# Performance work log

Hardware: AMD Instinct MI355X
Metric: run time of the kernel (lower is better)

## Reference

```python
import jax, jax.numpy as jnp
import numpy as np

B, FIN, FOUT, FH2, NMIX, LAT, H, W = 16, 256, 256, 256, 8, 512, 64, 64


def _xavier(key, shape):
    # xavier_normal_ over last-two-ish dims; simple fan-based scale
    fan_in = int(np.prod(shape[1:]))
    fan_out = shape[0]
    s = (2.0 / (fan_in + fan_out)) ** 0.5
    return jax.random.normal(key, shape, jnp.float32) * s


def setup_inputs() -> dict:
    key = jax.random.key(0)
    ks = jax.random.split(key, 12)
    return {
        "x": jax.random.normal(ks[0], (B, FIN, H, W), jnp.float32),
        "lat": jax.random.normal(ks[1], (B, LAT), jnp.float32),
        # mixture kernel banks [n_mix, out_ch, in_ch] (kernel_size=1 squeezed)
        "k_in_mix": _xavier(ks[2], (NMIX, FH2, FIN)),
        "k_mid_mix": _xavier(ks[3], (NMIX, FH2, 2 * FH2)),
        "k_out_mix": _xavier(ks[4], (NMIX, FOUT, 2 * FH2)),
        "k_short_mix": _xavier(ks[5], (NMIX, FOUT, FIN)),
        # mixture bias banks [n_mix, ch]
        "b_in_mix": _xavier(ks[6], (NMIX, FH2)),
        "b_mid_mix": _xavier(ks[7], (NMIX, FH2)),
        "b_out_mix": _xavier(ks[8], (NMIX, FOUT)),
        "b_short_mix": _xavier(ks[9], (NMIX, FOUT)),
        # dyna_mix = nn.Linear(lat_size, n_mix) (lat_factor=0 path)
        "w_dyna": _xavier(ks[10], (NMIX, LAT)),
        "b_dyna": jnp.zeros((NMIX,), jnp.float32),
    }


def _complex_wave(h):
    # doubles channel dim: concat(sin, cos) along channels (per sample)
    return jnp.concatenate([jnp.sin(h), jnp.cos(h)], axis=1)


def reference(x, lat, k_in_mix, k_mid_mix, k_out_mix, k_short_mix,
              b_in_mix, b_mid_mix, b_out_mix, b_short_mix, w_dyna, b_dyna):
    # mixing coefficients per sample: [B, n_mix]
    mix = lat @ w_dyna.T + b_dyna
    # per-sample 1x1 conv kernels via mixture reduction: [B, out, in]
    k_in = jnp.einsum('bm,moi->boi', mix, k_in_mix)
    k_mid = jnp.einsum('bm,moi->boi', mix, k_mid_mix)
    k_out = jnp.einsum('bm,moi->boi', mix, k_out_mix)
    k_short = jnp.einsum('bm,moi->boi', mix, k_short_mix)
    # per-sample biases: [B, ch, 1, 1]
    b_in = (mix @ b_in_mix)[:, :, None, None]
    b_mid = (mix @ b_mid_mix)[:, :, None, None]
    b_out = (mix @ b_out_mix)[:, :, None, None]
    b_short = (mix @ b_short_mix)[:, :, None, None]
    # grouped conv with groups = batch (kernel_size=1) == per-sample matmul
    short = jnp.einsum('boi,bihw->bohw', k_short, x) + b_short
    h = jnp.einsum('boi,bihw->bohw', k_in, x) + b_in            # [B, FH2, H, W]
    h = _complex_wave(h)                                        # [B, 2*FH2, H, W]
    h = jnp.einsum('boi,bihw->bohw', k_mid, h) + b_mid
    h = _complex_wave(h)
    out = jnp.einsum('boi,bihw->bohw', k_out, h) + b_out + short
    return out
```

## Files before the change

### kernel.cpp

```cpp
#include <hip/hip_runtime.h>
#include <stdint.h>

#define B_    16
#define FIN   256
#define FOUT  256
#define FH2   256
#define NMIX  8
#define LAT   512
#define HW    4096
#define MT    64

typedef short bf16x8 __attribute__((ext_vector_type(8)));
typedef float f32x4  __attribute__((ext_vector_type(4)));

#define WS_MIX    0
#define WS_BIAS   1024
#define WS_WIN    131072
#define WS_WMID   2228224
#define WS_WOUT   6422528
#define WS_WSHORT 10616832

__device__ __forceinline__ uint16_t f2bf(float f) {
  uint32_t u = __builtin_bit_cast(uint32_t, f);
  u += 0x7fffu + ((u >> 16) & 1u);
  return (uint16_t)(u >> 16);
}
__device__ __forceinline__ uint32_t pack2(float lo, float hi) {
  return (uint32_t)f2bf(lo) | ((uint32_t)f2bf(hi) << 16);
}

#define MFMA(a, b, c) __builtin_amdgcn_mfma_f32_16x16x32_bf16(a, b, c, 0, 0, 0)

__global__ void k_mix_bias(const float* __restrict__ lat,
                           const float* __restrict__ w_dyna,
                           const float* __restrict__ b_dyna,
                           const float* __restrict__ b_in_mix,
                           const float* __restrict__ b_mid_mix,
                           const float* __restrict__ b_out_mix,
                           const float* __restrict__ b_short_mix,
                           float* __restrict__ ws_mix,
                           float* __restrict__ ws_bias) {
  __shared__ float smix[NMIX];
  const int t = threadIdx.x;
  const int lane = t & 63, wv = t >> 6;
  const int b = blockIdx.x;
#pragma unroll
  for (int d2 = 0; d2 < 2; d2++) {
    int m = wv * 2 + d2;
    float s = 0.f;
#pragma unroll
    for (int j = 0; j < 8; j++)
      s += lat[b * LAT + j * 64 + lane] * w_dyna[m * LAT + j * 64 + lane];
#pragma unroll
    for (int off = 32; off; off >>= 1) s += __shfl_xor(s, off);
    if (lane == 0) {
      float v = s + b_dyna[m];
      ws_mix[b * NMIX + m] = v;
      smix[m] = v;
    }
  }
  __syncthreads();
  const float* banks[4] = {b_in_mix, b_mid_mix, b_out_mix, b_short_mix};
  for (int pos = t; pos < 1024; pos += 256) {
    int bank = pos >> 8, ch = pos & 255;
    const float* bp = banks[bank];
    float a = 0.f;
#pragma unroll
    for (int m = 0; m < NMIX; m++) a += smix[m] * bp[m * 256 + ch];
    ws_bias[(bank * B_ + b) * 256 + ch] = a;
  }
}

__global__ void k_weights(const float* __restrict__ k_in_mix,
                          const float* __restrict__ k_mid_mix,
                          const float* __restrict__ k_out_mix,
                          const float* __restrict__ k_short_mix,
                          const float* __restrict__ ws_mix,
                          uint16_t* __restrict__ w_in,
                          uint16_t* __restrict__ w_mid,
                          uint16_t* __restrict__ w_out,
                          uint16_t* __restrict__ w_short) {
  __shared__ float smix[B_ * NMIX];
  const int t = threadIdx.x;
  if (t < B_ * NMIX) smix[t] = ws_mix[t];
  __syncthreads();
  const int idx = blockIdx.x * 256 + t;
  const float* src;
  uint16_t* dst;
  int sstride, dstride;
  if (idx < 65536) {
    int e = idx;
    int j = e & 7, lane = (e >> 3) & 63, ots = (e >> 9) & 3, kt = (e >> 11) & 7, wv = e >> 14;
    int row = wv * 64 + ots * 16 + (lane & 15);
    int k = kt * 32 + (lane >> 4) * 8 + j;
    src = k_in_mix + row * 256 + k; sstride = 65536;
    dst = w_in + e;                 dstride = 65536;
  } else if (idx < 196608) {
    int e = idx - 65536;
    int j = e & 7, lane = (e >> 3) & 63, ots = (e >> 9) & 3, kt = (e >> 11) & 15, wv = e >> 15;
    int row = wv * 64 + ots * 16 + (lane & 15);
    int kp = kt * 32 + (lane >> 4) * 8 + j;
    int i = (kp >> 1) + ((kp & 1) << 8);
    src = k_mid_mix + row * 512 + i; sstride = 131072;
    dst = w_mid + e;                 dstride = 131072;
  } else if (idx < 327680) {
    int e = idx - 196608;
    int j = e & 7, lane = (e >> 3) & 63, ots = (e >> 9) & 3, kt = (e >> 11) & 15, wv = e >> 15;
    int row = wv * 64 + ots * 16 + (lane & 15);
    int kp = kt * 32 + (lane >> 4) * 8 + j;
    int i = (kp >> 1) + ((kp & 1) << 8);
    src = k_out_mix + row * 512 + i; sstride = 131072;
    dst = w_out + e;                 dstride = 131072;
  } else {
    int e = idx - 327680;
    int j = e & 7, lane = (e >> 3) & 63, ots = (e >> 9) & 3, kt = (e >> 11) & 7, wv = e >> 14;
    int row = wv * 64 + ots * 16 + (lane & 15);
    int k = kt * 32 + (lane >> 4) * 8 + j;
    src = k_short_mix + row * 256 + k; sstride = 65536;
    dst = w_short + e;                 dstride = 65536;
  }
  float v[NMIX];
#pragma unroll
  for (int m = 0; m < NMIX; m++) v[m] = src[m * sstride];
  for (int b = 0; b < B_; b++) {
    float a = 0.f;
#pragma unroll
    for (int m = 0; m < NMIX; m++) a += smix[b * NMIX + m] * v[m];
    dst[b * dstride] = f2bf(a);
  }
}

__launch_bounds__(256, 2)
__global__ void k_main(const float* __restrict__ x,
                       const float* __restrict__ ws_bias,
                       const uint16_t* __restrict__ w_in,
                       const uint16_t* __restrict__ w_mid,
                       const uint16_t* __restrict__ w_out,
                       const uint16_t* __restrict__ w_short,
                       float* __restrict__ out) {
  __shared__ int4 smem4[73728 / 16];
  char* lds = (char*)smem4;
  char* Xc = lds;
  char* H1 = lds + 8192;

  const int t = threadIdx.x;
  const int lane = t & 63;
  const int wv = t >> 6;
  const int q = lane >> 4;
  const int n = lane & 15;
  const int b = blockIdx.x & 15;
  const int p0 = (blockIdx.x >> 4) * MT;

  const float* xb = x + (size_t)b * FIN * HW + p0;
  const int xpos = t & 63;
  const int xcg = wv;

  {
    const float* xs = xb + (size_t)(xcg * 8) * HW + xpos;
    float v[8];
#pragma unroll
    for (int e = 0; e < 8; e++) v[e] = xs[(size_t)e * HW];
    *(int4*)(Xc + xpos * 64 + ((xcg ^ (xpos & 3)) * 16)) =
        make_int4((int)pack2(v[0], v[1]), (int)pack2(v[2], v[3]),
                  (int)pack2(v[4], v[5]), (int)pack2(v[6], v[7]));
  }

  f32x4 acc_h[4][4], acc_s[4][4];
#pragma unroll
  for (int ots = 0; ots < 4; ots++) {
    const int o = wv * 64 + ots * 16 + q * 4;
    const float4 vi = *(const float4*)&ws_bias[(0 * B_ + b) * 256 + o];
    const float4 vs = *(const float4*)&ws_bias[(3 * B_ + b) * 256 + o];
    f32x4 ah, asv;
    ah[0] = vi.x; ah[1] = vi.y; ah[2] = vi.z; ah[3] = vi.w;
    asv[0] = vs.x; asv[1] = vs.y; asv[2] = vs.z; asv[3] = vs.w;
#pragma unroll
    for (int pt = 0; pt < 4; pt++) { acc_h[ots][pt] = ah; acc_s[ots][pt] = asv; }
  }

  const uint16_t* Wi = w_in + (size_t)b * 65536 + wv * 16384 + lane * 8;
  const uint16_t* Ws = w_short + (size_t)b * 65536 + wv * 16384 + lane * 8;
  bf16x8 ai[2][4], asf[2][4];
#pragma unroll
  for (int ots = 0; ots < 4; ots++) {
    ai[0][ots] = *(const bf16x8*)(Wi + ots * 512);
    asf[0][ots] = *(const bf16x8*)(Ws + ots * 512);
  }
  __syncthreads();

#pragma unroll
  for (int kt = 0; kt < 8; kt++) {
    float xv[8];
    if (kt < 7) {
      const float* xs = xb + (size_t)((kt + 1) * 32 + xcg * 8) * HW + xpos;
#pragma unroll
      for (int e = 0; e < 8; e++) xv[e] = xs[(size_t)e * HW];
#pragma unroll
      for (int ots = 0; ots < 4; ots++) {
        ai[(kt + 1) & 1][ots] = *(const bf16x8*)(Wi + (kt + 1) * 2048 + ots * 512);
        asf[(kt + 1) & 1][ots] = *(const bf16x8*)(Ws + (kt + 1) * 2048 + ots * 512);
      }
    }
    const char* Xr = Xc + (kt & 1) * 4096;
    bf16x8 bf[4];
#pragma unroll
    for (int pt = 0; pt < 4; pt++) {
      const int p = pt * 16 + n;
      bf[pt] = *(const bf16x8*)(Xr + p * 64 + ((q ^ (p & 3)) * 16));
    }
#pragma unroll
    for (int ots = 0; ots < 4; ots++) {
#pragma unroll
      for (int pt = 0; pt < 4; pt++) {
        acc_h[ots][pt] = MFMA(ai[kt & 1][ots], bf[pt], acc_h[ots][pt]);
        acc_s[ots][pt] = MFMA(asf[kt & 1][ots], bf[pt], acc_s[ots][pt]);
      }
    }
    if (kt < 7) {
      *(int4*)(Xc + ((kt + 1) & 1) * 4096 + xpos * 64 + ((xcg ^ (xpos & 3)) * 16)) =
          make_int4((int)pack2(xv[0], xv[1]), (int)pack2(xv[2], xv[3]),
                    (int)pack2(xv[4], xv[5]), (int)pack2(xv[6], xv[7]));
      __syncthreads();
    }
  }

#pragma unroll
  for (int ots = 0; ots < 4; ots++) {
    const int ctile = (wv * 4 + ots) * 4 + q;
#pragma unroll
    for (int pt = 0; pt < 4; pt++) {
      const int p = pt * 16 + n;
      *(int4*)(H1 + p * 1024 + ((ctile ^ (p & 7)) * 16)) = make_int4(
          (int)pack2(__sinf(acc_h[ots][pt][0]), __cosf(acc_h[ots][pt][0])),
          (int)pack2(__sinf(acc_h[ots][pt][1]), __cosf(acc_h[ots][pt][1])),
          (int)pack2(__sinf(acc_h[ots][pt][2]), __cosf(acc_h[ots][pt][2])),
          (int)pack2(__sinf(acc_h[ots][pt][3]), __cosf(acc_h[ots][pt][3])));
    }
  }

  const uint16_t* Wm = w_mid + (size_t)b * 131072 + wv * 32768 + lane * 8;
  bf16x8 am[3][4];
#pragma unroll
  for (int ots = 0; ots < 4; ots++) {
    am[0][ots] = *(const bf16x8*)(Wm + ots * 512);
    am[1][ots] = *(const bf16x8*)(Wm + 2048 + ots * 512);
  }
  f32x4 acc2[4][4];
#pragma unroll
  for (int ots = 0; ots < 4; ots++) {
    const int o = wv * 64 + ots * 16 + q * 4;
    const float4 v = *(const float4*)&ws_bias[(1 * B_ + b) * 256 + o];
    f32x4 a2;
    a2[0] = v.x; a2[1] = v.y; a2[2] = v.z; a2[3] = v.w;
#pragma unroll
    for (int pt = 0; pt < 4; pt++) acc2[ots][pt] = a2;
  }
  __syncthreads();

#pragma unroll
  for (int kt = 0; kt < 16; kt++) {
    if (kt < 14) {
#pragma unroll
      for (int ots = 0; ots < 4; ots++)
        am[(kt + 2) % 3][ots] = *(const bf16x8*)(Wm + (kt + 2) * 2048 + ots * 512);
    }
    bf16x8 bf[4];
#pragma unroll
    for (int pt = 0; pt < 4; pt++) {
      const int p = pt * 16 + n;
      bf[pt] = *(const bf16x8*)(H1 + p * 1024 + (((kt * 4 + q) ^ (p & 7)) * 16));
    }
#pragma unroll
    for (int ots = 0; ots < 4; ots++)
#pragma unroll
      for (int pt = 0; pt < 4; pt++)
        acc2[ots][pt] = MFMA(am[kt % 3][ots], bf[pt], acc2[ots][pt]);
  }
  __syncthreads();

#pragma unroll
  for (int ots = 0; ots < 4; ots++) {
    const int ctile = (wv * 4 + ots) * 4 + q;
#pragma unroll
    for (int pt = 0; pt < 4; pt++) {
      const int p = pt * 16 + n;
      *(int4*)(H1 + p * 1024 + ((ctile ^ (p & 7)) * 16)) = make_int4(
          (int)pack2(__sinf(acc2[ots][pt][0]), __cosf(acc2[ots][pt][0])),
          (int)pack2(__sinf(acc2[ots][pt][1]), __cosf(acc2[ots][pt][1])),
          (int)pack2(__sinf(acc2[ots][pt][2]), __cosf(acc2[ots][pt][2])),
          (int)pack2(__sinf(acc2[ots][pt][3]), __cosf(acc2[ots][pt][3])));
    }
  }

  const uint16_t* Wo = w_out + (size_t)b * 131072 + wv * 32768 + lane * 8;
  bf16x8 ao[3][4];
#pragma unroll
  for (int ots = 0; ots < 4; ots++) {
    ao[0][ots] = *(const bf16x8*)(Wo + ots * 512);
    ao[1][ots] = *(const bf16x8*)(Wo + 2048 + ots * 512);
  }
#pragma unroll
  for (int ots = 0; ots < 4; ots++) {
    const int o = wv * 64 + ots * 16 + q * 4;
    const float4 v = *(const float4*)&ws_bias[(2 * B_ + b) * 256 + o];
#pragma unroll
    for (int pt = 0; pt < 4; pt++) {
      acc_s[ots][pt][0] += v.x; acc_s[ots][pt][1] += v.y;
      acc_s[ots][pt][2] += v.z; acc_s[ots][pt][3] += v.w;
    }
  }
  __syncthreads();

#pragma unroll
  for (int kt = 0; kt < 16; kt++) {
    if (kt < 14) {
#pragma unroll
      for (int ots = 0; ots < 4; ots++)
        ao[(kt + 2) % 3][ots] = *(const bf16x8*)(Wo + (kt + 2) * 2048 + ots * 512);
    }
    bf16x8 bf[4];
#pragma unroll
    for (int pt = 0; pt < 4; pt++) {
      const int p = pt * 16 + n;
      bf[pt] = *(const bf16x8*)(H1 + p * 1024 + (((kt * 4 + q) ^ (p & 7)) * 16));
    }
#pragma unroll
    for (int ots = 0; ots < 4; ots++)
#pragma unroll
      for (int pt = 0; pt < 4; pt++)
        acc_s[ots][pt] = MFMA(ao[kt % 3][ots], bf[pt], acc_s[ots][pt]);
  }

  {
    float* ob = out + (size_t)b * FOUT * HW + p0;
#pragma unroll
    for (int ots = 0; ots < 4; ots++) {
#pragma unroll
      for (int pt = 0; pt < 4; pt++) {
#pragma unroll
        for (int r = 0; r < 4; r++) {
          const int o = wv * 64 + ots * 16 + q * 4 + r;
          ob[(size_t)o * HW + pt * 16 + n] = acc_s[ots][pt][r];
        }
      }
    }
  }
}

extern "C" void kernel_launch(void* const* d_in, const int* in_sizes, int n_in,
                              void* d_out, int out_size, void* d_ws, size_t ws_size,
                              hipStream_t stream) {
  const float* x           = (const float*)d_in[0];
  const float* lat         = (const float*)d_in[1];
  const float* k_in_mix    = (const float*)d_in[2];
  const float* k_mid_mix   = (const float*)d_in[3];
  const float* k_out_mix   = (const float*)d_in[4];
  const float* k_short_mix = (const float*)d_in[5];
  const float* b_in_mix    = (const float*)d_in[6];
  const float* b_mid_mix   = (const float*)d_in[7];
  const float* b_out_mix   = (const float*)d_in[8];
  const float* b_short_mix = (const float*)d_in[9];
  const float* w_dyna      = (const float*)d_in[10];
  const float* b_dyna      = (const float*)d_in[11];

  char* ws = (char*)d_ws;
  float*    ws_mix  = (float*)(ws + WS_MIX);
  float*    ws_bias = (float*)(ws + WS_BIAS);
  uint16_t* w_in    = (uint16_t*)(ws + WS_WIN);
  uint16_t* w_mid   = (uint16_t*)(ws + WS_WMID);
  uint16_t* w_out   = (uint16_t*)(ws + WS_WOUT);
  uint16_t* w_short = (uint16_t*)(ws + WS_WSHORT);
  float* out = (float*)d_out;

  hipLaunchKernelGGL(k_mix_bias, dim3(16), dim3(256), 0, stream,
                     lat, w_dyna, b_dyna, b_in_mix, b_mid_mix, b_out_mix,
                     b_short_mix, ws_mix, ws_bias);
  hipLaunchKernelGGL(k_weights, dim3(1536), dim3(256), 0, stream,
                     k_in_mix, k_mid_mix, k_out_mix, k_short_mix, ws_mix,
                     w_in, w_mid, w_out, w_short);
  hipLaunchKernelGGL(k_main, dim3(1024), dim3(256), 0, stream,
                     x, ws_bias, w_in, w_mid, w_out, w_short, out);
}
```

Baseline: 207.5 us.

## Vectorize weight mixing and deepen prefetch pipelines with MFMA priority

The weight-mixing kernel now has each thread process 8 contiguous packed outputs. It reads float4 vectors and writes int4 packets, which cuts the grid from 1536 to 192 blocks and removes scalar strided accesses. The main kernel prefetches x two k-tiles ahead instead of one, and deepens the w_mid and w_out register prefetch from 3 to 4 stages. It also wraps the MFMA blocks in s_setprio to favour the matrix issue. The cost is higher register pressure under the 2-blocks-per-SM launch bound, which could cause spills or lower occupancy.

```diff
diff --git a/kernel.cpp b/kernel.cpp
--- a/kernel.cpp
+++ b/kernel.cpp
@@ -84,49 +84,64 @@
   const int t = threadIdx.x;
   if (t < B_ * NMIX) smix[t] = ws_mix[t];
   __syncthreads();
-  const int idx = blockIdx.x * 256 + t;
-  const float* src;
+  const int e8 = (blockIdx.x * 256 + t) * 8;
+  const float* srcA;
   uint16_t* dst;
   int sstride, dstride;
-  if (idx < 65536) {
-    int e = idx;
-    int j = e & 7, lane = (e >> 3) & 63, ots = (e >> 9) & 3, kt = (e >> 11) & 7, wv = e >> 14;
+  bool ileave;
+  if (e8 < 65536) {
+    int e = e8;
+    int lane = (e >> 3) & 63, ots = (e >> 9) & 3, kt = (e >> 11) & 7, wv = e >> 14;
     int row = wv * 64 + ots * 16 + (lane & 15);
-    int k = kt * 32 + (lane >> 4) * 8 + j;
-    src = k_in_mix + row * 256 + k; sstride = 65536;
-    dst = w_in + e;                 dstride = 65536;
-  } else if (idx < 196608) {
-    int e = idx - 65536;
-    int j = e & 7, lane = (e >> 3) & 63, ots = (e >> 9) & 3, kt = (e >> 11) & 15, wv = e >> 15;
+    int k0 = kt * 32 + (lane >> 4) * 8;
+    srcA = k_in_mix + row * 256 + k0; sstride = 65536; ileave = false;
+    dst = w_in + e;                   dstride = 65536;
+  } else if (e8 < 196608) {
+    int e = e8 - 65536;
+    int lane = (e >> 3) & 63, ots = (e >> 9) & 3, kt = (e >> 11) & 15, wv = e >> 15;
     int row = wv * 64 + ots * 16 + (lane & 15);
-    int kp = kt * 32 + (lane >> 4) * 8 + j;
-    int i = (kp >> 1) + ((kp & 1) << 8);
-    src = k_mid_mix + row * 512 + i; sstride = 131072;
-    dst = w_mid + e;                 dstride = 131072;
-  } else if (idx < 327680) {
-    int e = idx - 196608;
-    int j = e & 7, lane = (e >> 3) & 63, ots = (e >> 9) & 3, kt = (e >> 11) & 15, wv = e >> 15;
+    int kp0 = kt * 32 + (lane >> 4) * 8;
+    srcA = k_mid_mix + row * 512 + (kp0 >> 1); sstride = 131072; ileave = true;
+    dst = w_mid + e;                           dstride = 131072;
+  } else if (e8 < 327680) {
+    int e = e8 - 196608;
+    int lane = (e >> 3) & 63, ots = (e >> 9) & 3, kt = (e >> 11) & 15, wv = e >> 15;
     int row = wv * 64 + ots * 16 + (lane & 15);
-    int kp = kt * 32 + (lane >> 4) * 8 + j;
-    int i = (kp >> 1) + ((kp & 1) << 8);
-    src = k_out_mix + row * 512 + i; sstride = 131072;
-    dst = w_out + e;                 dstride = 131072;
+    int kp0 = kt * 32 + (lane >> 4) * 8;
+    srcA = k_out_mix + row * 512 + (kp0 >> 1); sstride = 131072; ileave = true;
+    dst = w_out + e;                           dstride = 131072;
   } else {
-    int e = idx - 327680;
-    int j = e & 7, lane = (e >> 3) & 63, ots = (e >> 9) & 3, kt = (e >> 11) & 7, wv = e >> 14;
+    int e = e8 - 327680;
+    int lane = (e >> 3) & 63, ots = (e >> 9) & 3, kt = (e >> 11) & 7, wv = e >> 14;
     int row = wv * 64 + ots * 16 + (lane & 15);
-    int k = kt * 32 + (lane >> 4) * 8 + j;
-    src = k_short_mix + row * 256 + k; sstride = 65536;
-    dst = w_short + e;                 dstride = 65536;
-  }
-  float v[NMIX];
-#pragma unroll
-  for (int m = 0; m < NMIX; m++) v[m] = src[m * sstride];
+    int k0 = kt * 32 + (lane >> 4) * 8;
+    srcA = k_short_mix + row * 256 + k0; sstride = 65536; ileave = false;
+    dst = w_short + e;                   dstride = 65536;
+  }
+  const int boff = ileave ? 256 : 4;
+  float4 va[NMIX], vb[NMIX];
+#pragma unroll
+  for (int m = 0; m < NMIX; m++) {
+    va[m] = *(const float4*)(srcA + m * sstride);
+    vb[m] = *(const float4*)(srcA + m * sstride + boff);
+  }
   for (int b = 0; b < B_; b++) {
-    float a = 0.f;
-#pragma unroll
-    for (int m = 0; m < NMIX; m++) a += smix[b * NMIX + m] * v[m];
-    dst[b * dstride] = f2bf(a);
+    float4 ra = make_float4(0.f, 0.f, 0.f, 0.f), rb = ra;
+#pragma unroll
+    for (int m = 0; m < NMIX; m++) {
+      const float s = smix[b * NMIX + m];
+      ra.x += s * va[m].x; ra.y += s * va[m].y; ra.z += s * va[m].z; ra.w += s * va[m].w;
+      rb.x += s * vb[m].x; rb.y += s * vb[m].y; rb.z += s * vb[m].z; rb.w += s * vb[m].w;
+    }
+    int4 pkt;
+    if (ileave) {
+      pkt = make_int4((int)pack2(ra.x, rb.x), (int)pack2(ra.y, rb.y),
+                      (int)pack2(ra.z, rb.z), (int)pack2(ra.w, rb.w));
+    } else {
+      pkt = make_int4((int)pack2(ra.x, ra.y), (int)pack2(ra.z, ra.w),
+                      (int)pack2(rb.x, rb.y), (int)pack2(rb.z, rb.w));
+    }
+    *(int4*)(dst + (size_t)b * dstride) = pkt;
   }
 }
 
@@ -155,15 +170,16 @@
   const int xpos = t & 63;
   const int xcg = wv;
 
-  {
-    const float* xs = xb + (size_t)(xcg * 8) * HW + xpos;
-    float v[8];
-#pragma unroll
-    for (int e = 0; e < 8; e++) v[e] = xs[(size_t)e * HW];
-    *(int4*)(Xc + xpos * 64 + ((xcg ^ (xpos & 3)) * 16)) =
-        make_int4((int)pack2(v[0], v[1]), (int)pack2(v[2], v[3]),
-                  (int)pack2(v[4], v[5]), (int)pack2(v[6], v[7]));
-  }
+  float xv[2][8];
+#pragma unroll
+  for (int e = 0; e < 8; e++)
+    xv[0][e] = xb[(size_t)(0 * 32 + xcg * 8 + e) * HW + xpos];
+#pragma unroll
+  for (int e = 0; e < 8; e++)
+    xv[1][e] = xb[(size_t)(1 * 32 + xcg * 8 + e) * HW + xpos];
+  *(int4*)(Xc + xpos * 64 + ((xcg ^ (xpos & 3)) * 16)) =
+      make_int4((int)pack2(xv[0][0], xv[0][1]), (int)pack2(xv[0][2], xv[0][3]),
+                (int)pack2(xv[0][4], xv[0][5]), (int)pack2(xv[0][6], xv[0][7]));
 
   f32x4 acc_h[4][4], acc_s[4][4];
 #pragma unroll
@@ -190,11 +206,12 @@
 
 #pragma unroll
   for (int kt = 0; kt < 8; kt++) {
-    float xv[8];
+    if (kt < 6) {
+      const float* xs = xb + (size_t)((kt + 2) * 32 + xcg * 8) * HW + xpos;
+#pragma unroll
+      for (int e = 0; e < 8; e++) xv[kt & 1][e] = xs[(size_t)e * HW];
+    }
     if (kt < 7) {
-      const float* xs = xb + (size_t)((kt + 1) * 32 + xcg * 8) * HW + xpos;
-#pragma unroll
-      for (int e = 0; e < 8; e++) xv[e] = xs[(size_t)e * HW];
 #pragma unroll
       for (int ots = 0; ots < 4; ots++) {
         ai[(kt + 1) & 1][ots] = *(const bf16x8*)(Wi + (kt + 1) * 2048 + ots * 512);
@@ -208,6 +225,7 @@
       const int p = pt * 16 + n;
       bf[pt] = *(const bf16x8*)(Xr + p * 64 + ((q ^ (p & 3)) * 16));
     }
+    __builtin_amdgcn_s_setprio(1);
 #pragma unroll
     for (int ots = 0; ots < 4; ots++) {
 #pragma unroll
@@ -216,10 +234,12 @@
         acc_s[ots][pt] = MFMA(asf[kt & 1][ots], bf[pt], acc_s[ots][pt]);
       }
     }
+    __builtin_amdgcn_s_setprio(0);
     if (kt < 7) {
-      *(int4*)(Xc + ((kt + 1) & 1) * 4096 + xpos * 64 + ((xcg ^ (xpos & 3)) * 16)) =
-          make_int4((int)pack2(xv[0], xv[1]), (int)pack2(xv[2], xv[3]),
-                    (int)pack2(xv[4], xv[5]), (int)pack2(xv[6], xv[7]));
+      const int s = (kt + 1) & 1;
+      *(int4*)(Xc + s * 4096 + xpos * 64 + ((xcg ^ (xpos & 3)) * 16)) =
+          make_int4((int)pack2(xv[s][0], xv[s][1]), (int)pack2(xv[s][2], xv[s][3]),
+                    (int)pack2(xv[s][4], xv[s][5]), (int)pack2(xv[s][6], xv[s][7]));
       __syncthreads();
     }
   }
@@ -239,11 +259,12 @@
   }
 
   const uint16_t* Wm = w_mid + (size_t)b * 131072 + wv * 32768 + lane * 8;
-  bf16x8 am[3][4];
-#pragma unroll
-  for (int ots = 0; ots < 4; ots++) {
-    am[0][ots] = *(const bf16x8*)(Wm + ots * 512);
-    am[1][ots] = *(const bf16x8*)(Wm + 2048 + ots * 512);
+  bf16x8 am[4][4];
+#pragma unroll
+  for (int ots = 0; ots < 4; ots++) {
+    am[0][ots] = *(const bf16x8*)(Wm + 0 * 2048 + ots * 512);
+    am[1][ots] = *(const bf16x8*)(Wm + 1 * 2048 + ots * 512);
+    am[2][ots] = *(const bf16x8*)(Wm + 2 * 2048 + ots * 512);
   }
   f32x4 acc2[4][4];
 #pragma unroll
@@ -259,10 +280,10 @@
 
 #pragma unroll
   for (int kt = 0; kt < 16; kt++) {
-    if (kt < 14) {
+    if (kt < 13) {
 #pragma unroll
       for (int ots = 0; ots < 4; ots++)
-        am[(kt + 2) % 3][ots] = *(const bf16x8*)(Wm + (kt + 2) * 2048 + ots * 512);
+        am[(kt + 3) & 3][ots] = *(const bf16x8*)(Wm + (kt + 3) * 2048 + ots * 512);
     }
     bf16x8 bf[4];
 #pragma unroll
@@ -270,11 +291,13 @@
       const int p = pt * 16 + n;
       bf[pt] = *(const bf16x8*)(H1 + p * 1024 + (((kt * 4 + q) ^ (p & 7)) * 16));
     }
+    __builtin_amdgcn_s_setprio(1);
 #pragma unroll
     for (int ots = 0; ots < 4; ots++)
 #pragma unroll
       for (int pt = 0; pt < 4; pt++)
-        acc2[ots][pt] = MFMA(am[kt % 3][ots], bf[pt], acc2[ots][pt]);
+        acc2[ots][pt] = MFMA(am[kt & 3][ots], bf[pt], acc2[ots][pt]);
+    __builtin_amdgcn_s_setprio(0);
   }
   __syncthreads();
 
@@ -293,11 +316,12 @@
   }
 
   const uint16_t* Wo = w_out + (size_t)b * 131072 + wv * 32768 + lane * 8;
-  bf16x8 ao[3][4];
-#pragma unroll
-  for (int ots = 0; ots < 4; ots++) {
-    ao[0][ots] = *(const bf16x8*)(Wo + ots * 512);
-    ao[1][ots] = *(const bf16x8*)(Wo + 2048 + ots * 512);
+  bf16x8 ao[4][4];
+#pragma unroll
+  for (int ots = 0; ots < 4; ots++) {
+    ao[0][ots] = *(const bf16x8*)(Wo + 0 * 2048 + ots * 512);
+    ao[1][ots] = *(const bf16x8*)(Wo + 1 * 2048 + ots * 512);
+    ao[2][ots] = *(const bf16x8*)(Wo + 2 * 2048 + ots * 512);
   }
 #pragma unroll
   for (int ots = 0; ots < 4; ots++) {
@@ -313,10 +337,10 @@
 
 #pragma unroll
   for (int kt = 0; kt < 16; kt++) {
-    if (kt < 14) {
+    if (kt < 13) {
 #pragma unroll
       for (int ots = 0; ots < 4; ots++)
-        ao[(kt + 2) % 3][ots] = *(const bf16x8*)(Wo + (kt + 2) * 2048 + ots * 512);
+        ao[(kt + 3) & 3][ots] = *(const bf16x8*)(Wo + (kt + 3) * 2048 + ots * 512);
     }
     bf16x8 bf[4];
 #pragma unroll
@@ -324,11 +348,13 @@
       const int p = pt * 16 + n;
       bf[pt] = *(const bf16x8*)(H1 + p * 1024 + (((kt * 4 + q) ^ (p & 7)) * 16));
     }
+    __builtin_amdgcn_s_setprio(1);
 #pragma unroll
     for (int ots = 0; ots < 4; ots++)
 #pragma unroll
       for (int pt = 0; pt < 4; pt++)
-        acc_s[ots][pt] = MFMA(ao[kt % 3][ots], bf[pt], acc_s[ots][pt]);
+        acc_s[ots][pt] = MFMA(ao[kt & 3][ots], bf[pt], acc_s[ots][pt]);
+    __builtin_amdgcn_s_setprio(0);
   }
 
   {
@@ -375,7 +401,7 @@
   hipLaunchKernelGGL(k_mix_bias, dim3(16), dim3(256), 0, stream,
                      lat, w_dyna, b_dyna, b_in_mix, b_mid_mix, b_out_mix,
                      b_short_mix, ws_mix, ws_bias);
-  hipLaunchKernelGGL(k_weights, dim3(1536), dim3(256), 0, stream,
+  hipLaunchKernelGGL(k_weights, dim3(192), dim3(256), 0, stream,
                      k_in_mix, k_mid_mix, k_out_mix, k_short_mix, ws_mix,
                      w_in, w_mid, w_out, w_short);
   hipLaunchKernelGGL(k_main, dim3(1024), dim3(256), 0, stream,
```

Measured after the change: 201.7 us. 2.8% less time.
